# Performance work log

Measured on AMD Instinct MI355X. Metric: run time of the kernel, lower is better.

The kernel has to match this reference:

```python
import jax, jax.numpy as jnp
import numpy as np

B, L, D, M = 8, 2048, 512, 256
D2, H = 2 * D, 4 * D  # attention d_model, FFN hidden
EPS = 1e-6


def setup_inputs() -> dict:
    key = jax.random.key(0)
    ks = jax.random.split(key, 16)
    s2 = 1.0 / np.sqrt(D2)
    sD = 1.0 / np.sqrt(D)
    sH = 1.0 / np.sqrt(H)
    f32 = jnp.float32
    return {
        "zr": jax.random.normal(ks[0], (B, L, D), f32),
        "zi": jax.random.normal(ks[1], (B, L, D), f32),
        "Wq": jax.random.normal(ks[2], (D2, D2), f32) * s2,
        "Wk": jax.random.normal(ks[3], (D2, D2), f32) * s2,
        "Wv": jax.random.normal(ks[4], (D2, D2), f32) * s2,
        "Wo": jax.random.normal(ks[5], (D2, D2), f32) * s2,
        "Wf": jax.random.normal(ks[6], (M, D2), f32),  # trainable random features (std normal, FAVOR+)
        "b_attn": jnp.zeros((D,), f32),
        "W1r": jax.random.normal(ks[7], (D, H), f32) * sD,
        "W1i": jax.random.normal(ks[8], (D, H), f32) * sD,
        "b1r": jnp.zeros((H,), f32),
        "b1i": jnp.zeros((H,), f32),
        "W2r": jax.random.normal(ks[9], (H, D), f32) * sH,
        "W2i": jax.random.normal(ks[10], (H, D), f32) * sH,
        "b2r": jnp.zeros((D,), f32),
        "b2i": jnp.zeros((D,), f32),
        "b_ffn": jnp.zeros((D,), f32),
    }


def modrelu(xr, xi, b):
    # ModReLU: relu(|z| + b) * z / |z|, per-channel bias b
    mag = jnp.sqrt(xr * xr + xi * xi + EPS)
    s = jax.nn.relu(mag + b) / mag
    return xr * s, xi * s


def _block(zr, zi, Wq, Wk, Wv, Wo, Wf, b_attn,
           W1r, W1i, b1r, b1i, W2r, W2i, b2r, b2i, b_ffn):
    # --- kernelized linear attention on real/imag concat [B,L,2D] ---
    x = jnp.concatenate([zr, zi], axis=-1)
    scl = D2 ** -0.25
    q = (x @ Wq) * scl
    k = (x @ Wk) * scl
    v = x @ Wv
    # FAVOR+ positive features: phi(u) = exp(Wf u - |u|^2/2) / sqrt(m)
    pq = q @ Wf.T - 0.5 * jnp.sum(q * q, axis=-1, keepdims=True)  # [B,L,M]
    pk = k @ Wf.T - 0.5 * jnp.sum(k * k, axis=-1, keepdims=True)
    phi_q = jnp.exp(pq - jax.lax.stop_gradient(jnp.max(pq, axis=-1, keepdims=True))) / np.sqrt(M)
    phi_k = jnp.exp(pk - jax.lax.stop_gradient(jnp.max(pk))) / np.sqrt(M)
    kv = jnp.einsum('blm,bld->bmd', phi_k, v)              # [B,M,2D]
    den = jnp.einsum('blm,bm->bl', phi_q, phi_k.sum(axis=1))  # [B,L]
    y = jnp.einsum('blm,bmd->bld', phi_q, kv) / (den[..., None] + EPS)
    y = y @ Wo
    yr, yi = y[..., :D], y[..., D:]
    # Add & Norm (ModReLU)
    zr, zi = modrelu(zr + yr, zi + yi, b_attn)
    # --- complex FFN: complex Linear -> CReLU -> complex Linear ---
    hr = zr @ W1r - zi @ W1i + b1r
    hi = zr @ W1i + zi @ W1r + b1i
    hr = jax.nn.relu(hr)
    hi = jax.nn.relu(hi)
    fr = hr @ W2r - hi @ W2i + b2r
    fi = hr @ W2i + hi @ W2r + b2i
    # Add & Norm (ModReLU)
    zr, zi = modrelu(zr + fr, zi + fi, b_ffn)
    return jnp.stack([zr, zi], axis=-1)  # [B,L,D,2]


def reference(zr, zi, Wq, Wk, Wv, Wo, Wf, b_attn,
              W1r, W1i, b1r, b1i, W2r, W2i, b2r, b2i, b_ffn):
    return _block(zr, zi, Wq, Wk, Wv, Wo, Wf, b_attn,
                  W1r, W1i, b1r, b1i, W2r, W2i, b2r, b2i, b_ffn)
```

## Files before the change

### kernel.cpp

```cpp
#include <hip/hip_runtime.h>
#include <math.h>

#define B_ 8
#define L_ 2048
#define D_ 512
#define M_ 256
#define D2_ 1024
#define H_ 2048
#define N_ 16384
#define EPS_ 1e-6f

typedef __attribute__((ext_vector_type(8))) short bf16x8;
typedef __attribute__((ext_vector_type(4))) float f32x4;
typedef unsigned short ushort_t;
typedef unsigned int uint_t;

#define WAITCNT_VM8 0x0F78
#define WAITCNT_VM4 0x0F74
#define WAITCNT_VM0 0x0F70

__device__ __forceinline__ ushort_t f2bf(float f) {
    uint_t u = __float_as_uint(f);
    u += 0x7FFFu + ((u >> 16) & 1u);
    return (ushort_t)(u >> 16);
}
__device__ __forceinline__ float bf2f(ushort_t u) {
    return __uint_as_float(((uint_t)u) << 16);
}
__device__ __forceinline__ void gload_lds16(const void* g, void* l) {
    __builtin_amdgcn_global_load_lds(
        (const __attribute__((address_space(1))) void*)g,
        (__attribute__((address_space(3))) void*)l, 16, 0, 0);
}

__global__ __launch_bounds__(256)
void gemm_mfma(const ushort_t* __restrict__ A, const ushort_t* __restrict__ Bm,
               void* __restrict__ Cp, int K, int lda, int ldb, int ldc,
               long long sA, long long sB, long long sC,
               int epi, float alpha, const float* __restrict__ aux,
               int auxStride, const float* __restrict__ bias, int obf)
{
    __shared__ ushort_t As[4][128 * 32];
    __shared__ ushort_t Bs[4][128 * 32];

    const int bz = blockIdx.z;
    A  += (long long)bz * sA;
    Bm += (long long)bz * sB;
    const int row0 = blockIdx.y * 128;
    const int col0 = blockIdx.x * 128;

    const int tid  = threadIdx.x;
    const int lane = tid & 63;
    const int wave = tid >> 6;
    const int wr = wave >> 1, wc = wave & 1;

    const int srow = tid >> 2;
    const int skol = (((tid & 3) ^ ((tid >> 3) & 3)) * 8);

    f32x4 acc[4][4];
    #pragma unroll
    for (int i = 0; i < 4; ++i)
        #pragma unroll
        for (int j = 0; j < 4; ++j)
            acc[i][j] = (f32x4){0.f, 0.f, 0.f, 0.f};

    const int fr = lane & 15;
    const int fq = lane >> 4;
    const int koff = ((fq ^ ((fr >> 1) & 3))) * 8;

    const int nT = K >> 5;

    auto issue = [&](int t) {
        const int buf = t & 3;
        const int k0 = t << 5;
        gload_lds16(A + (long long)(row0 + srow) * lda + k0 + skol,
                    &As[buf][(wave * 16) * 32]);
        gload_lds16(A + (long long)(row0 + 64 + srow) * lda + k0 + skol,
                    &As[buf][(64 + wave * 16) * 32]);
        gload_lds16(Bm + (long long)(col0 + srow) * ldb + k0 + skol,
                    &Bs[buf][(wave * 16) * 32]);
        gload_lds16(Bm + (long long)(col0 + 64 + srow) * ldb + k0 + skol,
                    &Bs[buf][(64 + wave * 16) * 32]);
    };

    issue(0);
    if (nT > 1) issue(1);
    for (int t = 0; t < nT; ++t) {
        if (t + 2 < nT) {
            issue(t + 2);
            __builtin_amdgcn_s_waitcnt(WAITCNT_VM8);
        } else if (t + 1 < nT) {
            __builtin_amdgcn_s_waitcnt(WAITCNT_VM4);
        } else {
            __builtin_amdgcn_s_waitcnt(WAITCNT_VM0);
        }
        __builtin_amdgcn_s_barrier();

        const int cur = t & 3;
        bf16x8 a[4], b[4];
        #pragma unroll
        for (int i = 0; i < 4; ++i)
            a[i] = *(const bf16x8*)&As[cur][(wr * 64 + i * 16 + fr) * 32 + koff];
        #pragma unroll
        for (int j = 0; j < 4; ++j)
            b[j] = *(const bf16x8*)&Bs[cur][(wc * 64 + j * 16 + fr) * 32 + koff];
        #pragma unroll
        for (int i = 0; i < 4; ++i)
            #pragma unroll
            for (int j = 0; j < 4; ++j)
                acc[i][j] = __builtin_amdgcn_mfma_f32_16x16x32_bf16(
                    a[i], b[j], acc[i][j], 0, 0, 0);
    }

    const int gr0 = row0 + wr * 64;
    const int gc0 = col0 + wc * 64;
    #pragma unroll
    for (int i = 0; i < 4; ++i) {
        #pragma unroll
        for (int r = 0; r < 4; ++r) {
            const int row = gr0 + i * 16 + fq * 4 + r;
            float raux = 0.f;
            if (epi == 1 || epi == 2) raux = aux[(long long)bz * auxStride + row];
            #pragma unroll
            for (int j = 0; j < 4; ++j) {
                const int col = gc0 + j * 16 + fr;
                float v = acc[i][j][r];
                if (epi == 0)      v *= alpha;
                else if (epi == 1) v -= 0.5f * raux;
                else if (epi == 2) v = v / (raux + EPS_);
                else if (epi == 5) v -= 0.5f * aux[(long long)bz * auxStride + col];
                else if (epi == 3) { v += bias[col]; v = v > 0.f ? v : 0.f; }
                else if (epi == 4) v += bias[col];
                const long long off = (long long)bz * sC + (long long)row * ldc + col;
                if (obf) ((ushort_t*)Cp)[off] = f2bf(v);
                else     ((float*)Cp)[off] = v;
            }
        }
    }
}


__global__ __launch_bounds__(256)
void transpose_cvt_sq(const float* __restrict__ W, ushort_t* __restrict__ out)
{
    __shared__ float S[32][33];
    const int tx = threadIdx.x & 31, ty = threadIdx.x >> 5;
    const int n0 = blockIdx.x * 32, k0 = blockIdx.y * 32;
    #pragma unroll
    for (int r = 0; r < 4; ++r)
        S[ty + 8 * r][tx] = W[(long long)(k0 + ty + 8 * r) * 1024 + n0 + tx];
    __syncthreads();
    #pragma unroll
    for (int r = 0; r < 4; ++r)
        out[(long long)(n0 + ty + 8 * r) * 1024 + k0 + tx] = f2bf(S[tx][ty + 8 * r]);
}

__global__ __launch_bounds__(256)
void build_wc1T(const float* __restrict__ W1r, const float* __restrict__ W1i,
                ushort_t* __restrict__ out)
{
    __shared__ float S[32][33];
    const int tx = threadIdx.x & 31, ty = threadIdx.x >> 5;
    const int i0 = blockIdx.x * 32, j0 = blockIdx.y * 32;
    #pragma unroll
    for (int r = 0; r < 4; ++r) {
        const int i = i0 + ty + 8 * r, j = j0 + tx;
        float v;
        if (j < H_) v = (i < D_) ? W1r[(long long)i * H_ + j]
                                 : -W1i[(long long)(i - D_) * H_ + j];
        else {
            const int jj = j - H_;
            v = (i < D_) ? W1i[(long long)i * H_ + jj]
                         : W1r[(long long)(i - D_) * H_ + jj];
        }
        S[tx][ty + 8 * r] = v;
    }
    __syncthreads();
    #pragma unroll
    for (int r = 0; r < 4; ++r)
        out[(long long)(j0 + ty + 8 * r) * 1024 + i0 + tx] = f2bf(S[ty + 8 * r][tx]);
}

__global__ __launch_bounds__(256)
void build_wc2T(const float* __restrict__ W2r, const float* __restrict__ W2i,
                ushort_t* __restrict__ out)
{
    __shared__ float S[32][33];
    const int tx = threadIdx.x & 31, ty = threadIdx.x >> 5;
    const int i0 = blockIdx.x * 32, j0 = blockIdx.y * 32;
    #pragma unroll
    for (int r = 0; r < 4; ++r) {
        const int i = i0 + ty + 8 * r, j = j0 + tx;
        float v;
        if (i < H_) v = (j < D_) ? W2r[(long long)i * D_ + j]
                                 : W2i[(long long)i * D_ + (j - D_)];
        else {
            const int ii = i - H_;
            v = (j < D_) ? -W2i[(long long)ii * D_ + j]
                         : W2r[(long long)ii * D_ + (j - D_)];
        }
        S[tx][ty + 8 * r] = v;
    }
    __syncthreads();
    #pragma unroll
    for (int r = 0; r < 4; ++r)
        out[(long long)(j0 + ty + 8 * r) * 4096 + i0 + tx] = f2bf(S[ty + 8 * r][tx]);
}

__global__ __launch_bounds__(256)
void build_bias(const float* __restrict__ b1r, const float* __restrict__ b1i,
                const float* __restrict__ b2r, const float* __restrict__ b2i,
                float* __restrict__ bc1, float* __restrict__ bc2)
{
    const int t = blockIdx.x * 256 + threadIdx.x;
    bc1[t] = (t < H_) ? b1r[t] : b1i[t - H_];
    if (t < D2_) bc2[t] = (t < D_) ? b2r[t] : b2i[t - D_];
}

__global__ __launch_bounds__(256)
void cvt_Wf(const float* __restrict__ Wf, ushort_t* __restrict__ out)
{
    const int t = blockIdx.x * 256 + threadIdx.x;
    out[t] = f2bf(Wf[t]);
}

__global__ __launch_bounds__(256)
void cvt_x(const float* __restrict__ zr, const float* __restrict__ zi,
           ushort_t* __restrict__ x)
{
    long long t = (long long)blockIdx.x * 256 + threadIdx.x;
    long long n = t >> 8;
    int j4 = (int)(t & 255) << 2;
    float4 v;
    if (j4 < D_) v = *(const float4*)(zr + n * D_ + j4);
    else         v = *(const float4*)(zi + n * D_ + (j4 - D_));
    uint2 o;
    o.x = (uint_t)f2bf(v.x) | ((uint_t)f2bf(v.y) << 16);
    o.y = (uint_t)f2bf(v.z) | ((uint_t)f2bf(v.w) << 16);
    *(uint2*)(x + n * D2_ + j4) = o;
}

__global__ __launch_bounds__(256)
void rowsumsq_bf(const ushort_t* __restrict__ A, float* __restrict__ out)
{
    const int wid = threadIdx.x >> 6, lane = threadIdx.x & 63;
    const long long row = (long long)blockIdx.x * 4 + wid;
    const ushort_t* a = A + row * D2_;
    float s = 0.f;
    #pragma unroll
    for (int h = 0; h < 2; ++h) {
        uint4 u = *(const uint4*)(a + h * 512 + lane * 8);
        const uint_t w[4] = {u.x, u.y, u.z, u.w};
        #pragma unroll
        for (int p = 0; p < 4; ++p) {
            float lo = bf2f((ushort_t)(w[p] & 0xffff));
            float hi = bf2f((ushort_t)(w[p] >> 16));
            s += lo * lo + hi * hi;
        }
    }
    #pragma unroll
    for (int off = 32; off; off >>= 1) s += __shfl_down(s, off, 64);
    if (lane == 0) out[row] = s;
}

__global__ __launch_bounds__(256)
void phi_rowmax_exp(const float* __restrict__ P, ushort_t* __restrict__ out)
{
    const long long row = blockIdx.x;
    const int t = threadIdx.x;
    const float v = P[row * M_ + t];
    float m = v;
    #pragma unroll
    for (int off = 32; off; off >>= 1) m = fmaxf(m, __shfl_down(m, off, 64));
    __shared__ float sm[4];
    const int wid = t >> 6, lane = t & 63;
    if (lane == 0) sm[wid] = m;
    __syncthreads();
    const float mm = fmaxf(fmaxf(sm[0], sm[1]), fmaxf(sm[2], sm[3]));
    out[row * M_ + t] = f2bf(expf(v - mm) * 0.0625f);
}

__global__ __launch_bounds__(256)
void gmax1(const float* __restrict__ P, float* __restrict__ part, int n)
{
    float m = -3.4e38f;
    for (long long i = (long long)blockIdx.x * 256 + threadIdx.x; i < n;
         i += (long long)gridDim.x * 256)
        m = fmaxf(m, P[i]);
    #pragma unroll
    for (int off = 32; off; off >>= 1) m = fmaxf(m, __shfl_down(m, off, 64));
    __shared__ float sm[4];
    const int wid = threadIdx.x >> 6, lane = threadIdx.x & 63;
    if (lane == 0) sm[wid] = m;
    __syncthreads();
    if (threadIdx.x == 0)
        part[blockIdx.x] = fmaxf(fmaxf(sm[0], sm[1]), fmaxf(sm[2], sm[3]));
}

__global__ __launch_bounds__(256)
void gmax2(float* __restrict__ red)
{
    float m = -3.4e38f;
    for (int i = threadIdx.x; i < 1024; i += 256) m = fmaxf(m, red[256 + i]);
    #pragma unroll
    for (int off = 32; off; off >>= 1) m = fmaxf(m, __shfl_down(m, off, 64));
    __shared__ float sm[4];
    const int wid = threadIdx.x >> 6, lane = threadIdx.x & 63;
    if (lane == 0) sm[wid] = m;
    __syncthreads();
    if (threadIdx.x == 0) red[0] = fmaxf(fmaxf(sm[0], sm[1]), fmaxf(sm[2], sm[3]));
}

__global__ __launch_bounds__(256)
void phikT_exp(const float* __restrict__ P, const float* __restrict__ red,
               ushort_t* __restrict__ out)
{
    const long long i = (long long)blockIdx.x * 256 + threadIdx.x;
    out[i] = f2bf(expf(P[i] - red[0]) * 0.0625f);
}

__global__ __launch_bounds__(256)
void ksum_k(const ushort_t* __restrict__ phikT, float* __restrict__ ks)
{
    const int b = blockIdx.x >> 8, m = blockIdx.x & 255;
    const ushort_t* p = phikT + (long long)m * N_ + b * L_;
    uint4 u = *(const uint4*)(p + threadIdx.x * 8);
    const uint_t w[4] = {u.x, u.y, u.z, u.w};
    float s = 0.f;
    #pragma unroll
    for (int q = 0; q < 4; ++q)
        s += bf2f((ushort_t)(w[q] & 0xffff)) + bf2f((ushort_t)(w[q] >> 16));
    #pragma unroll
    for (int off = 32; off; off >>= 1) s += __shfl_down(s, off, 64);
    __shared__ float sm[4];
    const int wid = threadIdx.x >> 6, lane = threadIdx.x & 63;
    if (lane == 0) sm[wid] = s;
    __syncthreads();
    if (threadIdx.x == 0)
        ks[blockIdx.x] = sm[0] + sm[1] + sm[2] + sm[3];
}

__global__ __launch_bounds__(256)
void den_k(const ushort_t* __restrict__ phiq, const float* __restrict__ ks,
           float* __restrict__ den)
{
    const int wid = threadIdx.x >> 6, lane = threadIdx.x & 63;
    const long long n = (long long)blockIdx.x * 4 + wid;
    const int b = (int)(n >> 11);
    uint2 u = *(const uint2*)(phiq + n * M_ + lane * 4);
    float4 kk = *(const float4*)(ks + b * M_ + lane * 4);
    float s = bf2f((ushort_t)(u.x & 0xffff)) * kk.x
            + bf2f((ushort_t)(u.x >> 16)) * kk.y
            + bf2f((ushort_t)(u.y & 0xffff)) * kk.z
            + bf2f((ushort_t)(u.y >> 16)) * kk.w;
    #pragma unroll
    for (int off = 32; off; off >>= 1) s += __shfl_down(s, off, 64);
    if (lane == 0) den[n] = s;
}

__global__ __launch_bounds__(256)
void modrelu_attn(const float* __restrict__ zr, const float* __restrict__ zi,
                  const float* __restrict__ yo, const float* __restrict__ b_attn,
                  ushort_t* __restrict__ zst)
{
    const long long t = (long long)blockIdx.x * 256 + threadIdx.x;
    const long long n = t >> 9; const int d = (int)(t & 511);
    const float ar = zr[t] + yo[n * D2_ + d];
    const float ai = zi[t] + yo[n * D2_ + D_ + d];
    const float mag = sqrtf(ar * ar + ai * ai + EPS_);
    const float s = fmaxf(mag + b_attn[d], 0.f) / mag;
    zst[n * D2_ + d]      = f2bf(ar * s);
    zst[n * D2_ + D_ + d] = f2bf(ai * s);
}

__global__ __launch_bounds__(256)
void modrelu_out(const ushort_t* __restrict__ zst, const float* __restrict__ f,
                 const float* __restrict__ b_ffn, float* __restrict__ out)
{
    const long long t = (long long)blockIdx.x * 256 + threadIdx.x;
    const long long n = t >> 9; const int d = (int)(t & 511);
    const float ar = bf2f(zst[n * D2_ + d])      + f[n * D2_ + d];
    const float ai = bf2f(zst[n * D2_ + D_ + d]) + f[n * D2_ + D_ + d];
    const float mag = sqrtf(ar * ar + ai * ai + EPS_);
    const float s = fmaxf(mag + b_ffn[d], 0.f) / mag;
    out[t * 2]     = ar * s;
    out[t * 2 + 1] = ai * s;
}

extern "C" void kernel_launch(void* const* d_in, const int* in_sizes, int n_in,
                              void* d_out, int out_size, void* d_ws, size_t ws_size,
                              hipStream_t stream)
{
    const float* zr    = (const float*)d_in[0];
    const float* zi    = (const float*)d_in[1];
    const float* Wq    = (const float*)d_in[2];
    const float* Wk    = (const float*)d_in[3];
    const float* Wv    = (const float*)d_in[4];
    const float* Wo    = (const float*)d_in[5];
    const float* Wf    = (const float*)d_in[6];
    const float* b_attn= (const float*)d_in[7];
    const float* W1r   = (const float*)d_in[8];
    const float* W1i   = (const float*)d_in[9];
    const float* b1r   = (const float*)d_in[10];
    const float* b1i   = (const float*)d_in[11];
    const float* W2r   = (const float*)d_in[12];
    const float* W2i   = (const float*)d_in[13];
    const float* b2r   = (const float*)d_in[14];
    const float* b2i   = (const float*)d_in[15];
    const float* b_ffn = (const float*)d_in[16];

    char* w = (char*)d_ws;
    ushort_t* Xbf = (ushort_t*)(w + 0LL);
    ushort_t* A1  = (ushort_t*)(w + 33554432LL);
    float*    P   = (float*)   (w + 67108864LL);
    ushort_t* WqT = (ushort_t*)(w + 83886080LL);
    ushort_t* WkT = (ushort_t*)(w + 85983232LL);
    ushort_t* WvT = (ushort_t*)(w + 88080384LL);
    ushort_t* Wfb = (ushort_t*)(w + 90177536LL);
    ushort_t* F1  = (ushort_t*)(w + 100663296LL);
    ushort_t* F2  = (ushort_t*)(w + 109051904LL);
    ushort_t* WoT = (ushort_t*)(w + 117440512LL);
    ushort_t* KVT = (ushort_t*)(w + 119537664LL);
    float* ssqq = (float*)(w + 123731968LL);
    float* ssqk = (float*)(w + 123797504LL);
    float* den  = (float*)(w + 123863040LL);
    float* ksum = (float*)(w + 123928576LL);
    float* red  = (float*)(w + 123936768LL);

    const bool big = ws_size >= 152000000ULL;
    const int  RCH = big ? 8192 : 4096;
    ushort_t* Hb = (ushort_t*)(w + 33554432LL);
    float* Fb  = big ? (float*)(w + 117440512LL) : (float*)(w + 67108864LL);
    float* bc1 = big ? (float*)(w + 150994944LL) : (float*)(w + 123944960LL);
    float* bc2 = big ? (float*)(w + 151011328LL) : (float*)(w + 123961344LL);

    const float scl = 0.1767766952966369f;
    dim3 blk(256);

    auto GM = [&](const ushort_t* A, const ushort_t* Bm, void* C,
                  int rows, int cols, int K, int lda, int ldb, int ldc,
                  long long sA, long long sB, long long sC, int nb,
                  int epi, float alpha, const float* aux, int auxStride,
                  const float* bias, int obf) {
        dim3 grid(cols / 128, rows / 128, nb);
        gemm_mfma<<<grid, blk, 0, stream>>>(A, Bm, C, K, lda, ldb, ldc,
                                            sA, sB, sC, epi, alpha, aux,
                                            auxStride, bias, obf);
    };

    transpose_cvt_sq<<<dim3(32, 32), blk, 0, stream>>>(Wq, WqT);
    transpose_cvt_sq<<<dim3(32, 32), blk, 0, stream>>>(Wk, WkT);
    transpose_cvt_sq<<<dim3(32, 32), blk, 0, stream>>>(Wv, WvT);
    transpose_cvt_sq<<<dim3(32, 32), blk, 0, stream>>>(Wo, WoT);
    cvt_Wf<<<1024, blk, 0, stream>>>(Wf, Wfb);
    build_bias<<<16, blk, 0, stream>>>(b1r, b1i, b2r, b2i, bc1, bc2);
    cvt_x<<<N_ * (D2_ / 4) / 256, blk, 0, stream>>>(zr, zi, Xbf);

    GM(Xbf, WqT, A1, N_, D2_, D2_, D2_, D2_, D2_, 0, 0, 0, 1, 0, scl, nullptr, 0, nullptr, 1);
    rowsumsq_bf<<<N_ / 4, blk, 0, stream>>>(A1, ssqq);
    GM(A1, Wfb, P, N_, M_, D2_, D2_, D2_, M_, 0, 0, 0, 1, 1, 1.f, ssqq, 0, nullptr, 0);
    phi_rowmax_exp<<<N_, blk, 0, stream>>>(P, F1);

    GM(Xbf, WkT, A1, N_, D2_, D2_, D2_, D2_, D2_, 0, 0, 0, 1, 0, scl, nullptr, 0, nullptr, 1);
    rowsumsq_bf<<<N_ / 4, blk, 0, stream>>>(A1, ssqk);
    GM(Wfb, A1, P, M_, N_, D2_, D2_, D2_, N_, 0, 0, 0, 1, 5, 1.f, ssqk, 0, nullptr, 0);
    gmax1<<<1024, blk, 0, stream>>>(P, red + 256, M_ * N_);
    gmax2<<<1, blk, 0, stream>>>(red);
    phikT_exp<<<M_ * N_ / 256, blk, 0, stream>>>(P, red, F2);

    GM(WvT, Xbf, A1, D2_, N_, D2_, D2_, D2_, N_, 0, 0, 0, 1, 0, 1.f, nullptr, 0, nullptr, 1);

    ksum_k<<<B_ * M_, blk, 0, stream>>>(F2, ksum);
    GM(A1, F2, KVT, D2_, M_, L_, N_, N_, M_, L_, L_, (long long)D2_ * M_, B_,
       0, 1.f, nullptr, 0, nullptr, 1);

    den_k<<<N_ / 4, blk, 0, stream>>>(F1, ksum, den);
    GM(F1, KVT, A1, L_, D2_, M_, M_, M_, D2_, (long long)L_ * M_,
       (long long)D2_ * M_, (long long)L_ * D2_, B_, 2, 1.f, den, L_, nullptr, 1);

    for (int c = 0; c < 2; ++c) {
        const long long ro = (long long)c * 8192;
        GM(A1 + ro * D2_, WoT, P, 8192, D2_, D2_, D2_, D2_, D2_, 0, 0, 0, 1,
           0, 1.f, nullptr, 0, nullptr, 0);
        modrelu_attn<<<8192 * D_ / 256, blk, 0, stream>>>(
            zr + ro * D_, zi + ro * D_, P, b_attn, Xbf + ro * D2_);
    }

    build_wc1T<<<dim3(32, 128), blk, 0, stream>>>(W1r, W1i, F1);
    build_wc2T<<<dim3(128, 32), blk, 0, stream>>>(W2r, W2i, F2);

    for (int c = 0; c < N_ / RCH; ++c) {
        const long long ro = (long long)c * RCH;
        GM(Xbf + ro * D2_, F1, Hb, RCH, 2 * H_, D2_, D2_, D2_, 2 * H_,
           0, 0, 0, 1, 3, 1.f, nullptr, 0, bc1, 1);
        GM(Hb, F2, Fb, RCH, D2_, 2 * H_, 2 * H_, 2 * H_, D2_,
           0, 0, 0, 1, 4, 1.f, nullptr, 0, bc2, 0);
        modrelu_out<<<RCH * D_ / 256, blk, 0, stream>>>(
            Xbf + ro * D2_, Fb, b_ffn, (float*)d_out + ro * D2_);
    }

    (void)in_sizes; (void)n_in; (void)out_size;
}
```

Measured before the change: 1.149 ms.

## Add 256x256-tile 8-wave MFMA GEMM with interleaved staging for large GEMMs

Adds a 512-thread GEMM kernel with 256x256 output tiles, a double-buffered LDS ring, and quarter-tile global-to-LDS prefetches interleaved between MFMA phases under s_setprio. The launcher dispatches to it when rows, cols and K fit and the grid has at least 128 workgroups, and falls back to the 128x128 kernel otherwise. Larger tiles raise data reuse per LDS byte and cut global traffic. In exchange they use 128KB of LDS and many accumulator registers, which lowers occupancy and leaves tail-wave imbalance on some shapes.

Result: faster. 1.115 ms (-3.0%).

```diff
diff --git a/kernel.cpp b/kernel.cpp
--- a/kernel.cpp
+++ b/kernel.cpp
@@ -16,6 +16,7 @@
 typedef unsigned int uint_t;
 
 #define WAITCNT_VM8 0x0F78
+#define WAITCNT_VM6 0x0F76
 #define WAITCNT_VM4 0x0F74
 #define WAITCNT_VM0 0x0F70
 
@@ -139,6 +140,196 @@
     }
 }
 
+__global__ __launch_bounds__(512, 2)
+void gemm256(const ushort_t* __restrict__ A, const ushort_t* __restrict__ Bm,
+             void* __restrict__ Cp, int K, int lda, int ldb, int ldc,
+             long long sA, long long sB, long long sC,
+             int epi, float alpha, const float* __restrict__ aux,
+             int auxStride, const float* __restrict__ bias, int obf)
+{
+    __shared__ ushort_t As[2][256 * 64];
+    __shared__ ushort_t Bs[2][256 * 64];
+
+    const int bz = blockIdx.z;
+    A  += (long long)bz * sA;
+    Bm += (long long)bz * sB;
+    const int row0 = blockIdx.y * 256;
+    const int col0 = blockIdx.x * 256;
+
+    const int tid  = threadIdx.x;
+    const int lane = tid & 63;
+    const int wave = tid >> 6;
+    const int wr   = wave >> 2;
+    const int wcn  = wave & 3;
+
+    const int rloc  = tid >> 3;
+    const int csrc8 = (((tid & 7) ^ (rloc & 7)) << 3);
+
+    const int fr = lane & 15;
+    const int fq = lane >> 4;
+    const int sw = fr & 7;
+    const int c0off = ((fq ^ sw) << 3);
+    const int c1off = (((4 | fq) ^ sw) << 3);
+
+    const int nT = K >> 6;
+
+    f32x4 acc[8][4];
+    #pragma unroll
+    for (int i = 0; i < 8; ++i)
+        #pragma unroll
+        for (int j = 0; j < 4; ++j)
+            acc[i][j] = (f32x4){0.f, 0.f, 0.f, 0.f};
+
+    bf16x8 a[4][2];
+    bf16x8 b[4][2];
+
+    auto stage = [&](int bufS, int tS, int half) {
+        const int k0 = tS << 6;
+        const int rh = (half >= 2) ? 1 : 0;
+        const bool isA = (half == 0 || half == 3);
+        const ushort_t* g = isA
+            ? A  + (long long)(row0 + rh * 128 + rloc) * lda + k0 + csrc8
+            : Bm + (long long)(col0 + rh * 128 + rloc) * ldb + k0 + csrc8;
+        const long long gstep = 64LL * (isA ? lda : ldb);
+        ushort_t* l = (isA ? &As[bufS][0] : &Bs[bufS][0])
+                      + (rh * 128 + wave * 8) * 64;
+        gload_lds16(g, l);
+        gload_lds16(g + gstep, l + 64 * 64);
+    };
+
+    auto ldsA = [&](int buf, int mh, int i, int koff) -> bf16x8 {
+        return *(const bf16x8*)
+            &As[buf][(wr * 128 + mh * 64 + i * 16 + fr) * 64 + koff];
+    };
+    auto ldsB = [&](int buf, int j, int koff) -> bf16x8 {
+        return *(const bf16x8*)
+            &Bs[buf][(wcn * 64 + j * 16 + fr) * 64 + koff];
+    };
+
+    stage(0, 0, 0); stage(0, 0, 1); stage(0, 0, 2); stage(0, 0, 3);
+    stage(1, 1, 0); stage(1, 1, 1); stage(1, 1, 2);
+    __builtin_amdgcn_s_waitcnt(WAITCNT_VM6);
+    __builtin_amdgcn_s_barrier();
+
+    auto tile_body = [&](int t, int buf) {
+        #pragma unroll
+        for (int i = 0; i < 4; ++i) {
+            a[i][0] = ldsA(buf, 0, i, c0off);
+            a[i][1] = ldsA(buf, 0, i, c1off);
+        }
+        #pragma unroll
+        for (int j = 0; j < 2; ++j) {
+            b[j][0] = ldsB(buf, j, c0off);
+            b[j][1] = ldsB(buf, j, c1off);
+        }
+        if (t + 1 < nT) stage(buf ^ 1, t + 1, 3);
+        __builtin_amdgcn_s_barrier();
+        asm volatile("s_waitcnt lgkmcnt(0)" ::: "memory");
+        __builtin_amdgcn_s_setprio(1);
+        #pragma unroll
+        for (int i = 0; i < 4; ++i)
+            #pragma unroll
+            for (int j = 0; j < 2; ++j) {
+                acc[i][j] = __builtin_amdgcn_mfma_f32_16x16x32_bf16(
+                    a[i][0], b[j][0], acc[i][j], 0, 0, 0);
+                acc[i][j] = __builtin_amdgcn_mfma_f32_16x16x32_bf16(
+                    a[i][1], b[j][1], acc[i][j], 0, 0, 0);
+            }
+        __builtin_amdgcn_s_setprio(0);
+        __builtin_amdgcn_s_barrier();
+
+        #pragma unroll
+        for (int j = 2; j < 4; ++j) {
+            b[j][0] = ldsB(buf, j, c0off);
+            b[j][1] = ldsB(buf, j, c1off);
+        }
+        __builtin_amdgcn_s_barrier();
+        asm volatile("s_waitcnt lgkmcnt(0)" ::: "memory");
+        __builtin_amdgcn_s_setprio(1);
+        #pragma unroll
+        for (int i = 0; i < 4; ++i)
+            #pragma unroll
+            for (int j = 2; j < 4; ++j) {
+                acc[i][j] = __builtin_amdgcn_mfma_f32_16x16x32_bf16(
+                    a[i][0], b[j][0], acc[i][j], 0, 0, 0);
+                acc[i][j] = __builtin_amdgcn_mfma_f32_16x16x32_bf16(
+                    a[i][1], b[j][1], acc[i][j], 0, 0, 0);
+            }
+        __builtin_amdgcn_s_setprio(0);
+        __builtin_amdgcn_s_barrier();
+
+        #pragma unroll
+        for (int i = 0; i < 4; ++i) {
+            a[i][0] = ldsA(buf, 1, i, c0off);
+            a[i][1] = ldsA(buf, 1, i, c1off);
+        }
+        if (t + 2 < nT) stage(buf, t + 2, 1);
+        __builtin_amdgcn_s_barrier();
+        asm volatile("s_waitcnt lgkmcnt(0)" ::: "memory");
+        __builtin_amdgcn_s_setprio(1);
+        #pragma unroll
+        for (int i = 0; i < 4; ++i)
+            #pragma unroll
+            for (int j = 2; j < 4; ++j) {
+                acc[4 + i][j] = __builtin_amdgcn_mfma_f32_16x16x32_bf16(
+                    a[i][0], b[j][0], acc[4 + i][j], 0, 0, 0);
+                acc[4 + i][j] = __builtin_amdgcn_mfma_f32_16x16x32_bf16(
+                    a[i][1], b[j][1], acc[4 + i][j], 0, 0, 0);
+            }
+        __builtin_amdgcn_s_setprio(0);
+        __builtin_amdgcn_s_barrier();
+
+        if (t + 2 < nT) { stage(buf, t + 2, 2); stage(buf, t + 2, 0); }
+        __builtin_amdgcn_s_barrier();
+        asm volatile("s_waitcnt lgkmcnt(0)" ::: "memory");
+        __builtin_amdgcn_s_setprio(1);
+        #pragma unroll
+        for (int i = 0; i < 4; ++i)
+            #pragma unroll
+            for (int j = 0; j < 2; ++j) {
+                acc[4 + i][j] = __builtin_amdgcn_mfma_f32_16x16x32_bf16(
+                    a[i][0], b[j][0], acc[4 + i][j], 0, 0, 0);
+                acc[4 + i][j] = __builtin_amdgcn_mfma_f32_16x16x32_bf16(
+                    a[i][1], b[j][1], acc[4 + i][j], 0, 0, 0);
+            }
+        __builtin_amdgcn_s_setprio(0);
+        if (t + 2 < nT)      __builtin_amdgcn_s_waitcnt(WAITCNT_VM6);
+        else if (t + 1 < nT) __builtin_amdgcn_s_waitcnt(WAITCNT_VM0);
+        __builtin_amdgcn_s_barrier();
+    };
+
+    for (int t = 0; t < nT; t += 2) {
+        tile_body(t, 0);
+        tile_body(t + 1, 1);
+    }
+
+    const int gr0 = row0 + wr * 128;
+    const int gc0 = col0 + wcn * 64;
+    #pragma unroll
+    for (int i = 0; i < 8; ++i) {
+        #pragma unroll
+        for (int r = 0; r < 4; ++r) {
+            const int row = gr0 + i * 16 + fq * 4 + r;
+            float raux = 0.f;
+            if (epi == 1 || epi == 2) raux = aux[(long long)bz * auxStride + row];
+            #pragma unroll
+            for (int j = 0; j < 4; ++j) {
+                const int col = gc0 + j * 16 + fr;
+                float v = acc[i][j][r];
+                if (epi == 0)      v *= alpha;
+                else if (epi == 1) v -= 0.5f * raux;
+                else if (epi == 2) v = v / (raux + EPS_);
+                else if (epi == 5) v -= 0.5f * aux[(long long)bz * auxStride + col];
+                else if (epi == 3) { v += bias[col]; v = v > 0.f ? v : 0.f; }
+                else if (epi == 4) v += bias[col];
+                const long long off = (long long)bz * sC + (long long)row * ldc + col;
+                if (obf) ((ushort_t*)Cp)[off] = f2bf(v);
+                else     ((float*)Cp)[off] = v;
+            }
+        }
+    }
+}
+
 
 __global__ __launch_bounds__(256)
 void transpose_cvt_sq(const float* __restrict__ W, ushort_t* __restrict__ out)
@@ -442,10 +633,19 @@
                   long long sA, long long sB, long long sC, int nb,
                   int epi, float alpha, const float* aux, int auxStride,
                   const float* bias, int obf) {
-        dim3 grid(cols / 128, rows / 128, nb);
-        gemm_mfma<<<grid, blk, 0, stream>>>(A, Bm, C, K, lda, ldb, ldc,
-                                            sA, sB, sC, epi, alpha, aux,
-                                            auxStride, bias, obf);
+        const long long wg256 = (long long)(cols >> 8) * (rows >> 8) * nb;
+        if ((rows & 255) == 0 && (cols & 255) == 0 && (K & 127) == 0 &&
+            wg256 >= 128) {
+            dim3 grid(cols / 256, rows / 256, nb);
+            gemm256<<<grid, dim3(512), 0, stream>>>(A, Bm, C, K, lda, ldb, ldc,
+                                                    sA, sB, sC, epi, alpha, aux,
+                                                    auxStride, bias, obf);
+        } else {
+            dim3 grid(cols / 128, rows / 128, nb);
+            gemm_mfma<<<grid, blk, 0, stream>>>(A, Bm, C, K, lda, ldb, ldc,
+                                                sA, sB, sC, epi, alpha, aux,
+                                                auxStride, bias, obf);
+        }
     };
 
     transpose_cvt_sq<<<dim3(32, 32), blk, 0, stream>>>(Wq, WqT);
```

## Switch GEMM K-loop from 4-stage to double-buffered LDS pipeline

Applied to the files above, without the earlier changes.

Replaces the four-buffer, prefetch-distance-two LDS pipeline in the bf16 MFMA GEMM with a two-buffer ping-pong scheme. Each step prefetches only one tile ahead, and a second barrier after the MFMAs guards buffer reuse. The loop is unrolled by two with fixed buffer pointers, and LDS use per block is halved, which may allow more resident blocks. In exchange, memory latency is hidden less deeply and there is an extra barrier per iteration. The t+=2 loop also assumes nT is even.

Measured after the change: 1.202 ms. 1.05x slower.

```diff
diff --git a/kernel.cpp b/kernel.cpp
--- a/kernel.cpp
+++ b/kernel.cpp
@@ -15,7 +15,6 @@
 typedef unsigned short ushort_t;
 typedef unsigned int uint_t;
 
-#define WAITCNT_VM8 0x0F78
 #define WAITCNT_VM4 0x0F74
 #define WAITCNT_VM0 0x0F70
 
@@ -40,8 +39,8 @@
                int epi, float alpha, const float* __restrict__ aux,
                int auxStride, const float* __restrict__ bias, int obf)
 {
-    __shared__ ushort_t As[4][128 * 32];
-    __shared__ ushort_t Bs[4][128 * 32];
+    __shared__ ushort_t As[2][128 * 32];
+    __shared__ ushort_t Bs[2][128 * 32];
 
     const int bz = blockIdx.z;
     A  += (long long)bz * sA;
@@ -70,46 +69,48 @@
 
     const int nT = K >> 5;
 
-    auto issue = [&](int t) {
-        const int buf = t & 3;
+    auto issue = [&](int t, ushort_t* Ad, ushort_t* Bd) {
         const int k0 = t << 5;
         gload_lds16(A + (long long)(row0 + srow) * lda + k0 + skol,
-                    &As[buf][(wave * 16) * 32]);
+                    Ad + (wave * 16) * 32);
         gload_lds16(A + (long long)(row0 + 64 + srow) * lda + k0 + skol,
-                    &As[buf][(64 + wave * 16) * 32]);
+                    Ad + (64 + wave * 16) * 32);
         gload_lds16(Bm + (long long)(col0 + srow) * ldb + k0 + skol,
-                    &Bs[buf][(wave * 16) * 32]);
+                    Bd + (wave * 16) * 32);
         gload_lds16(Bm + (long long)(col0 + 64 + srow) * ldb + k0 + skol,
-                    &Bs[buf][(64 + wave * 16) * 32]);
+                    Bd + (64 + wave * 16) * 32);
     };
 
-    issue(0);
-    if (nT > 1) issue(1);
-    for (int t = 0; t < nT; ++t) {
-        if (t + 2 < nT) {
-            issue(t + 2);
-            __builtin_amdgcn_s_waitcnt(WAITCNT_VM8);
-        } else if (t + 1 < nT) {
+    auto body = [&](int t, const ushort_t* Ac, const ushort_t* Bc,
+                    ushort_t* An, ushort_t* Bn) {
+        if (t + 1 < nT) {
+            issue(t + 1, An, Bn);
             __builtin_amdgcn_s_waitcnt(WAITCNT_VM4);
         } else {
             __builtin_amdgcn_s_waitcnt(WAITCNT_VM0);
         }
         __builtin_amdgcn_s_barrier();
 
-        const int cur = t & 3;
         bf16x8 a[4], b[4];
         #pragma unroll
         for (int i = 0; i < 4; ++i)
-            a[i] = *(const bf16x8*)&As[cur][(wr * 64 + i * 16 + fr) * 32 + koff];
+            a[i] = *(const bf16x8*)&Ac[(wr * 64 + i * 16 + fr) * 32 + koff];
         #pragma unroll
         for (int j = 0; j < 4; ++j)
-            b[j] = *(const bf16x8*)&Bs[cur][(wc * 64 + j * 16 + fr) * 32 + koff];
+            b[j] = *(const bf16x8*)&Bc[(wc * 64 + j * 16 + fr) * 32 + koff];
         #pragma unroll
         for (int i = 0; i < 4; ++i)
             #pragma unroll
             for (int j = 0; j < 4; ++j)
                 acc[i][j] = __builtin_amdgcn_mfma_f32_16x16x32_bf16(
                     a[i], b[j], acc[i][j], 0, 0, 0);
+        __builtin_amdgcn_s_barrier();
+    };
+
+    issue(0, As[0], Bs[0]);
+    for (int t = 0; t < nT; t += 2) {
+        body(t,     As[0], Bs[0], As[1], Bs[1]);
+        body(t + 1, As[1], Bs[1], As[0], Bs[0]);
     }
 
     const int gr0 = row0 + wr * 64;
```
